# Kernel optimization log

Hardware: AMD Instinct MI355X
Metric: run time of the kernel (lower is better)

The kernel has to match this reference:

```python
import jax, jax.numpy as jnp
import numpy as np

B, C, H, W = 8, 512, 64, 64
DEPTH, HEADS = 4, 8


def setup_inputs() -> dict:
    key = jax.random.key(0)
    ks = jax.random.split(key, 7)
    s = 0.02
    return {
        "x": jax.random.normal(ks[0], (B, C, H, W), jnp.float32),
        # axial positional embeddings, emb dim at index 1: (1,C,H,1) and (1,C,1,W)
        "pos_h": jax.random.normal(ks[1], (C, H), jnp.float32) * s,
        "pos_w": jax.random.normal(ks[2], (C, W), jnp.float32) * s,
        # per layer, per axis (0=height, 1=width): q, kv, out projections
        "wq": jax.random.normal(ks[3], (DEPTH, 2, C, C), jnp.float32) * s,
        "wkv": jax.random.normal(ks[4], (DEPTH, 2, C, 2 * C), jnp.float32) * s,
        "wo": jax.random.normal(ks[5], (DEPTH, 2, C, C), jnp.float32) * s,
        "wo_b": jax.random.normal(ks[6], (DEPTH, 2, C), jnp.float32) * s,
    }


def _attn_last_axis(x, wq, wkv, wo, wo_b, heads):
    """Self-attention along the second-to-last axis. x: (..., L, C)."""
    lead = x.shape[:-2]
    L, Cd = x.shape[-2], x.shape[-1]
    e = Cd // heads
    q = x @ wq                       # (..., L, C)
    k, v = jnp.split(x @ wkv, 2, axis=-1)
    sh = lead + (L, heads, e)
    q, k, v = q.reshape(sh), k.reshape(sh), v.reshape(sh)
    dots = jnp.einsum('...ihe,...jhe->...hij', q, k) * (e ** -0.5)
    attn = jax.nn.softmax(dots, axis=-1)
    out = jnp.einsum('...hij,...jhe->...ihe', attn, v).reshape(lead + (L, heads * e))
    return out @ wo + wo_b


def reference(x, pos_h, pos_w, wq, wkv, wo, wo_b):
    # positional embedding: x + (1,C,H,1) + (1,C,1,W)
    x = x + pos_h[None, :, :, None] + pos_w[None, :, None, :]
    y = jnp.transpose(x, (0, 2, 3, 1))  # (B,H,W,C) channels-last working layout
    for l in range(DEPTH):
        # height-axis attention: (B,W,H,C), attend along H
        yh = jnp.transpose(y, (0, 2, 1, 3))
        oh = _attn_last_axis(yh, wq[l, 0], wkv[l, 0], wo[l, 0], wo_b[l, 0], HEADS)
        oh = jnp.transpose(oh, (0, 2, 1, 3))
        # width-axis attention: attend along W
        ow = _attn_last_axis(y, wq[l, 1], wkv[l, 1], wo[l, 1], wo_b[l, 1], HEADS)
        y = oh + ow  # sum_axial_out=True, no residual
    return jnp.transpose(y, (0, 3, 1, 2))  # back to (B,C,H,W)
```

## Files before the change

### kernel.cpp

```cpp
#include <hip/hip_runtime.h>
#include <stdint.h>


typedef __attribute__((ext_vector_type(8))) short bf16x8;
typedef __attribute__((ext_vector_type(4))) float f32x4;
typedef unsigned short u16;
typedef unsigned int u32;

#define MFMA16(a, b, c) __builtin_amdgcn_mfma_f32_16x16x32_bf16((a), (b), (c), 0, 0, 0)

__device__ __forceinline__ float b2f(u16 h) {
    u32 u = ((u32)h) << 16;
    float f;
    __builtin_memcpy(&f, &u, 4);
    return f;
}
__device__ __forceinline__ u16 f2b(float f) {
    u32 u;
    __builtin_memcpy(&u, &f, 4);
    u32 r = (u + 0x7fffu + ((u >> 16) & 1u)) >> 16;
    return (u16)r;
}

#define GLD_LDS16(g, l)                                                        \
    __builtin_amdgcn_global_load_lds(                                          \
        (const __attribute__((address_space(1))) void*)(g),                    \
        (__attribute__((address_space(3))) void*)(l), 16, 0, 0)

__global__ __launch_bounds__(256) void embed_kernel(
    const float* __restrict__ x, const float* __restrict__ ph,
    const float* __restrict__ pw, u16* __restrict__ y)
{
    __shared__ float tile[64][65];
    const int c0 = blockIdx.x * 64, h = blockIdx.y, b = blockIdx.z;
    const int t = threadIdx.x;
#pragma unroll
    for (int i = 0; i < 4; ++i) {
        int cl = (t >> 4) + i * 16;
        int w4 = (t & 15) * 4;
        const float* src = x + (((size_t)(b * 512 + c0 + cl)) * 64 + h) * 64 + w4;
        float4 v = *(const float4*)src;
        float p = ph[(c0 + cl) * 64 + h];
        tile[cl][w4 + 0] = v.x + p + pw[(c0 + cl) * 64 + w4 + 0];
        tile[cl][w4 + 1] = v.y + p + pw[(c0 + cl) * 64 + w4 + 1];
        tile[cl][w4 + 2] = v.z + p + pw[(c0 + cl) * 64 + w4 + 2];
        tile[cl][w4 + 3] = v.w + p + pw[(c0 + cl) * 64 + w4 + 3];
    }
    __syncthreads();
    const int wl = t >> 2, cb = (t & 3) * 16;
    bf16x8 o0, o1;
#pragma unroll
    for (int j = 0; j < 8; ++j) o0[j] = (short)f2b(tile[cb + j][wl]);
#pragma unroll
    for (int j = 0; j < 8; ++j) o1[j] = (short)f2b(tile[cb + 8 + j][wl]);
    u16* dst = y + (((size_t)(b * 64 + h) * 64 + wl) * 512 + c0 + cb);
    *(bf16x8*)dst = o0;
    *(bf16x8*)(dst + 8) = o1;
}

__global__ __launch_bounds__(256) void wtrans_kernel(
    const float* __restrict__ wq, const float* __restrict__ wkv,
    const float* __restrict__ wo, u16* __restrict__ wT)
{
    const int mid = blockIdx.z;
    const int l = mid / 6, rest = mid % 6, axis = rest / 3, which = rest % 3;
    const size_t la = (size_t)(l * 2 + axis);
    const float* src;
    int N;
    size_t doff;
    if (which == 0)      { src = wq  + la * 512 * 512;  N = 512;  doff = la * (2048 * 512); }
    else if (which == 1) { src = wkv + la * 512 * 1024; N = 1024; doff = la * (2048 * 512) + 512 * 512; }
    else                 { src = wo  + la * 512 * 512;  N = 512;  doff = la * (2048 * 512) + 512 * 512 + 1024 * 512; }
    const int n0 = blockIdx.y * 64;
    if (n0 >= N) return;
    const int k0 = blockIdx.x * 64;
    __shared__ float tile[64][65];
    const int t = threadIdx.x;
#pragma unroll
    for (int i = 0; i < 4; ++i) {
        int kl = (t >> 4) + i * 16;
        int n4 = (t & 15) * 4;
        float4 v = *(const float4*)(src + (size_t)(k0 + kl) * N + n0 + n4);
        tile[kl][n4 + 0] = v.x; tile[kl][n4 + 1] = v.y;
        tile[kl][n4 + 2] = v.z; tile[kl][n4 + 3] = v.w;
    }
    __syncthreads();
    const int nl = t >> 2, kb = (t & 3) * 16;
    bf16x8 o0, o1;
#pragma unroll
    for (int j = 0; j < 8; ++j) o0[j] = (short)f2b(tile[kb + j][nl]);
#pragma unroll
    for (int j = 0; j < 8; ++j) o1[j] = (short)f2b(tile[kb + 8 + j][nl]);
    u16* dst = wT + doff + (size_t)(n0 + nl) * 512 + k0 + kb;
    *(bf16x8*)dst = o0;
    *(bf16x8*)(dst + 8) = o1;
}

template <int MODE>
__global__ __launch_bounds__(256) void gemm_bt(
    const u16* __restrict__ A, int lda,
    const u16* __restrict__ Bt,
    const float* __restrict__ bias,
    u16* C, int ldc)
{
    __shared__ u16 As[128 * 64];
    __shared__ u16 Bs[128 * 64];
    const int tid = threadIdx.x;
    const int lane = tid & 63;
    const int wv = tid >> 6;
    const int wr = (wv >> 1) * 64, wc = (wv & 1) * 64;
    const int m0 = blockIdx.x * 128;
    const int n0 = blockIdx.y * 128;
    const int rl = lane >> 3;
    const int cp = lane & 7;
    const int l16 = lane & 15;
    const int kgrp = (lane >> 4) << 3;
    f32x4 acc[4][4] = {};

    for (int ks = 0; ks < 512; ks += 64) {
#pragma unroll
        for (int i = 0; i < 4; ++i) {
            int row = wv * 8 + i * 32 + rl;
            int clog = cp ^ (row & 7);
            const u16* src = A + (size_t)(m0 + row) * lda + ks + clog * 8;
            GLD_LDS16(src, As + (wv * 8 + i * 32) * 64);
        }
#pragma unroll
        for (int i = 0; i < 4; ++i) {
            int row = wv * 8 + i * 32 + rl;
            int clog = cp ^ (row & 7);
            const u16* src = Bt + (size_t)(n0 + row) * 512 + ks + clog * 8;
            GLD_LDS16(src, Bs + (wv * 8 + i * 32) * 64);
        }
        __syncthreads();
#pragma unroll
        for (int kk = 0; kk < 2; ++kk) {
            bf16x8 af[4], bfr[4];
            const int kb = (kk * 32 + kgrp) * 2;
#pragma unroll
            for (int mf = 0; mf < 4; ++mf) {
                int row = wr + mf * 16 + l16;
                af[mf] = *(const bf16x8*)((const char*)As + row * 128 + (kb ^ ((row & 7) << 4)));
            }
#pragma unroll
            for (int nf = 0; nf < 4; ++nf) {
                int row = wc + nf * 16 + l16;
                bfr[nf] = *(const bf16x8*)((const char*)Bs + row * 128 + (kb ^ ((row & 7) << 4)));
            }
#pragma unroll
            for (int mf = 0; mf < 4; ++mf)
#pragma unroll
                for (int nf = 0; nf < 4; ++nf)
                    acc[mf][nf] = MFMA16(af[mf], bfr[nf], acc[mf][nf]);
        }
        __syncthreads();
    }

    float bv[4];
    if (MODE >= 1) {
#pragma unroll
        for (int nf = 0; nf < 4; ++nf) bv[nf] = bias[n0 + wc + nf * 16 + l16];
    }
#pragma unroll
    for (int mf = 0; mf < 4; ++mf) {
#pragma unroll
        for (int r = 0; r < 4; ++r) {
            int m = m0 + wr + mf * 16 + ((lane >> 4) << 2) + r;
#pragma unroll
            for (int nf = 0; nf < 4; ++nf) {
                int n = n0 + wc + nf * 16 + l16;
                float v = acc[mf][nf][r];
                if (MODE >= 1) v += bv[nf];
                if (MODE == 2) v += b2f(C[(size_t)m * ldc + n]);
                C[(size_t)m * ldc + n] = f2b(v);
            }
        }
    }
}

__global__ __launch_bounds__(256) void attn_kernel(u16* QKV, int bstr, int tstr)
{
    __shared__ u16 sm[4][2][64 * 64];
    const int bi = blockIdx.x;
    const int base = (bi >> 6) * 4096 + (bi & 63) * bstr;
    const int tid = threadIdx.x, lane = tid & 63, wv = tid >> 6;
    const int l16 = lane & 15, kgrp = (lane >> 4) << 3;
    const int rl = lane >> 3, cp = lane & 7;
    u16* Kl = (u16*)sm[wv][0];
    u16* Vt = (u16*)sm[wv][1];

    for (int hh = 0; hh < 2; ++hh) {
        const int head = wv + hh * 4;
        const int hoff = head * 64;

        bf16x8 q[4][2];
#pragma unroll
        for (int mf = 0; mf < 4; ++mf)
#pragma unroll
            for (int k2 = 0; k2 < 2; ++k2) {
                const u16* p = QKV + (size_t)(base + (mf * 16 + l16) * tstr) * 1536
                             + hoff + k2 * 32 + kgrp;
                q[mf][k2] = *(const bf16x8*)p;
            }
        bf16x8 vvr[8];
#pragma unroll
        for (int i = 0; i < 8; ++i) {
            int j = i * 8 + rl;
            vvr[i] = *(const bf16x8*)(QKV + (size_t)(base + j * tstr) * 1536 + 1024 + hoff + cp * 8);
        }
#pragma unroll
        for (int i = 0; i < 8; ++i) {
            int row = i * 8 + rl;
            int clog = cp ^ (row & 7);
            const u16* src = QKV + (size_t)(base + row * tstr) * 1536 + 512 + hoff + clog * 8;
            GLD_LDS16(src, Kl + i * 8 * 64);
        }
        __syncthreads();

        f32x4 dt[4][4] = {};
#pragma unroll
        for (int k2 = 0; k2 < 2; ++k2) {
            bf16x8 bfr[4];
            const int kb = (k2 * 32 + kgrp) * 2;
#pragma unroll
            for (int jf = 0; jf < 4; ++jf) {
                int row = jf * 16 + l16;
                bfr[jf] = *(const bf16x8*)((const char*)Kl + row * 128 + (kb ^ ((row & 7) << 4)));
            }
#pragma unroll
            for (int mf = 0; mf < 4; ++mf)
#pragma unroll
                for (int jf = 0; jf < 4; ++jf)
                    dt[mf][jf] = MFMA16(q[mf][k2], bfr[jf], dt[mf][jf]);
        }

#pragma unroll
        for (int mf = 0; mf < 4; ++mf) {
#pragma unroll
            for (int r = 0; r < 4; ++r) {
                float a0 = dt[mf][0][r] * 0.125f, a1 = dt[mf][1][r] * 0.125f;
                float a2 = dt[mf][2][r] * 0.125f, a3 = dt[mf][3][r] * 0.125f;
                float mx = fmaxf(fmaxf(a0, a1), fmaxf(a2, a3));
#pragma unroll
                for (int msk = 1; msk < 16; msk <<= 1) mx = fmaxf(mx, __shfl_xor(mx, msk, 64));
                float e0 = __expf(a0 - mx), e1 = __expf(a1 - mx);
                float e2 = __expf(a2 - mx), e3 = __expf(a3 - mx);
                float sum = e0 + e1 + e2 + e3;
#pragma unroll
                for (int msk = 1; msk < 16; msk <<= 1) sum += __shfl_xor(sum, msk, 64);
                float inv = __builtin_amdgcn_rcpf(sum);
                dt[mf][0][r] = e0 * inv; dt[mf][1][r] = e1 * inv;
                dt[mf][2][r] = e2 * inv; dt[mf][3][r] = e3 * inv;
            }
        }

#pragma unroll
        for (int i = 0; i < 8; ++i) {
            int j = i * 8 + rl;
#pragma unroll
            for (int t = 0; t < 8; ++t) {
                int e = cp * 8 + t;
                int addr = e * 128 + 2 * j;
                *(u16*)((char*)Vt + (addr ^ ((e & 7) << 4))) = (u16)vvr[i][t];
            }
        }
#pragma unroll
        for (int mf = 0; mf < 4; ++mf)
#pragma unroll
            for (int r = 0; r < 4; ++r) {
                int irow = mf * 16 + ((lane >> 4) << 2) + r;
#pragma unroll
                for (int jf = 0; jf < 4; ++jf) {
                    int j = jf * 16 + l16;
                    int addr = irow * 128 + 2 * j;
                    *(u16*)((char*)Kl + (addr ^ ((irow & 7) << 4))) = f2b(dt[mf][jf][r]);
                }
            }

        f32x4 o[4][4] = {};
#pragma unroll
        for (int k2 = 0; k2 < 2; ++k2) {
            bf16x8 af[4], bfr[4];
            const int kb = (k2 * 32 + kgrp) * 2;
#pragma unroll
            for (int mf = 0; mf < 4; ++mf) {
                int row = mf * 16 + l16;
                af[mf] = *(const bf16x8*)((const char*)Kl + row * 128 + (kb ^ ((row & 7) << 4)));
            }
#pragma unroll
            for (int ef = 0; ef < 4; ++ef) {
                int row = ef * 16 + l16;
                bfr[ef] = *(const bf16x8*)((const char*)Vt + row * 128 + (kb ^ ((row & 7) << 4)));
            }
#pragma unroll
            for (int mf = 0; mf < 4; ++mf)
#pragma unroll
                for (int ef = 0; ef < 4; ++ef)
                    o[mf][ef] = MFMA16(af[mf], bfr[ef], o[mf][ef]);
        }

#pragma unroll
        for (int mf = 0; mf < 4; ++mf)
#pragma unroll
            for (int r = 0; r < 4; ++r) {
                int irow = mf * 16 + ((lane >> 4) << 2) + r;
                size_t rowoff = (size_t)(base + irow * tstr) * 1536;
#pragma unroll
                for (int ef = 0; ef < 4; ++ef) {
                    int e = ef * 16 + l16;
                    QKV[rowoff + hoff + e] = f2b(o[mf][ef][r]);
                }
            }
        __syncthreads();
    }
}

__global__ __launch_bounds__(256) void untrans_kernel(
    const u16* __restrict__ y, float* __restrict__ out)
{
    __shared__ float tile[64][65];
    const int c0 = blockIdx.x * 64, h = blockIdx.y, b = blockIdx.z;
    const int t = threadIdx.x;
    {
        const int wl = t >> 2, cb = (t & 3) * 16;
        const u16* src = y + (((size_t)(b * 64 + h) * 64 + wl) * 512 + c0 + cb);
        bf16x8 v0 = *(const bf16x8*)src;
        bf16x8 v1 = *(const bf16x8*)(src + 8);
#pragma unroll
        for (int j = 0; j < 8; ++j) tile[wl][cb + j] = b2f((u16)v0[j]);
#pragma unroll
        for (int j = 0; j < 8; ++j) tile[wl][cb + 8 + j] = b2f((u16)v1[j]);
    }
    __syncthreads();
    const int cl = t >> 2, w16 = (t & 3) * 16;
    float* dst = out + (((size_t)(b * 512 + c0 + cl)) * 64 + h) * 64 + w16;
#pragma unroll
    for (int j = 0; j < 4; ++j) {
        float4 v;
        v.x = tile[w16 + j * 4 + 0][cl];
        v.y = tile[w16 + j * 4 + 1][cl];
        v.z = tile[w16 + j * 4 + 2][cl];
        v.w = tile[w16 + j * 4 + 3][cl];
        *(float4*)(dst + j * 4) = v;
    }
}

extern "C" void kernel_launch(void* const* d_in, const int* in_sizes, int n_in,
                              void* d_out, int out_size, void* d_ws, size_t ws_size,
                              hipStream_t stream)
{
    (void)in_sizes; (void)n_in; (void)out_size; (void)ws_size;
    const float* x   = (const float*)d_in[0];
    const float* ph  = (const float*)d_in[1];
    const float* pw  = (const float*)d_in[2];
    const float* wq  = (const float*)d_in[3];
    const float* wkv = (const float*)d_in[4];
    const float* wo  = (const float*)d_in[5];
    const float* wob = (const float*)d_in[6];

    char* ws = (char*)d_ws;
    u16* yA  = (u16*)(ws);
    u16* yB  = (u16*)(ws + 33554432);
    u16* QKV = (u16*)(ws + 67108864);
    u16* wT  = (u16*)(ws + 167772160);
    float* out = (float*)d_out;

    embed_kernel<<<dim3(8, 64, 8), 256, 0, stream>>>(x, ph, pw, yA);
    wtrans_kernel<<<dim3(8, 16, 24), 256, 0, stream>>>(wq, wkv, wo, wT);

    u16* yin = yA;
    u16* yout = yB;
    for (int l = 0; l < 4; ++l) {
        for (int axis = 0; axis < 2; ++axis) {
            const u16* wTla = wT + (size_t)(l * 2 + axis) * 2048 * 512;
            const float* bias = wob + (size_t)(l * 2 + axis) * 512;
            gemm_bt<0><<<dim3(256, 12), 256, 0, stream>>>(yin, 512, wTla, nullptr, QKV, 1536);
            int bstr = (axis == 0) ? 1 : 64;
            int tstr = (axis == 0) ? 64 : 1;
            attn_kernel<<<dim3(512), 256, 0, stream>>>(QKV, bstr, tstr);
            const u16* woT = wTla + 512 * 512 + 1024 * 512;
            if (axis == 0)
                gemm_bt<1><<<dim3(256, 4), 256, 0, stream>>>(QKV, 1536, woT, bias, yout, 512);
            else
                gemm_bt<2><<<dim3(256, 4), 256, 0, stream>>>(QKV, 1536, woT, bias, yout, 512);
        }
        u16* tmp = yin; yin = yout; yout = tmp;
    }
    untrans_kernel<<<dim3(8, 64, 8), 256, 0, stream>>>(yin, out);
}
```

Before: 1.284 ms.

## Transpose MFMA operands for vectorized epilogues, XCD-aware block remap, and drop attention syncthreads

```diff
diff --git a/kernel.cpp b/kernel.cpp
--- a/kernel.cpp
+++ b/kernel.cpp
@@ -109,12 +109,17 @@
     const int lane = tid & 63;
     const int wv = tid >> 6;
     const int wr = (wv >> 1) * 64, wc = (wv & 1) * 64;
-    const int m0 = blockIdx.x * 128;
-    const int n0 = blockIdx.y * 128;
+    const int nbx = gridDim.x;
+    int lin = blockIdx.x + nbx * blockIdx.y;
+    int cpx = (nbx * gridDim.y) >> 3;
+    int id = (lin & 7) * cpx + (lin >> 3);
+    const int n0 = (id % nbx) * 128;
+    const int m0 = (id / nbx) * 128;
     const int rl = lane >> 3;
     const int cp = lane & 7;
     const int l16 = lane & 15;
-    const int kgrp = (lane >> 4) << 3;
+    const int g = lane >> 4;
+    const int kgrp = g << 3;
     f32x4 acc[4][4] = {};
 
     for (int ks = 0; ks < 512; ks += 64) {
@@ -148,32 +153,40 @@
                 bfr[nf] = *(const bf16x8*)((const char*)Bs + row * 128 + (kb ^ ((row & 7) << 4)));
             }
 #pragma unroll
-            for (int mf = 0; mf < 4; ++mf)
-#pragma unroll
-                for (int nf = 0; nf < 4; ++nf)
-                    acc[mf][nf] = MFMA16(af[mf], bfr[nf], acc[mf][nf]);
+            for (int nf = 0; nf < 4; ++nf)
+#pragma unroll
+                for (int mf = 0; mf < 4; ++mf)
+                    acc[nf][mf] = MFMA16(bfr[nf], af[mf], acc[nf][mf]);
         }
         __syncthreads();
     }
 
-    float bv[4];
+    float bv[4][4];
     if (MODE >= 1) {
 #pragma unroll
-        for (int nf = 0; nf < 4; ++nf) bv[nf] = bias[n0 + wc + nf * 16 + l16];
+        for (int nf = 0; nf < 4; ++nf) {
+            float4 b4 = *(const float4*)(bias + n0 + wc + nf * 16 + g * 4);
+            bv[nf][0] = b4.x; bv[nf][1] = b4.y; bv[nf][2] = b4.z; bv[nf][3] = b4.w;
+        }
     }
 #pragma unroll
     for (int mf = 0; mf < 4; ++mf) {
-#pragma unroll
-        for (int r = 0; r < 4; ++r) {
-            int m = m0 + wr + mf * 16 + ((lane >> 4) << 2) + r;
-#pragma unroll
-            for (int nf = 0; nf < 4; ++nf) {
-                int n = n0 + wc + nf * 16 + l16;
-                float v = acc[mf][nf][r];
-                if (MODE >= 1) v += bv[nf];
-                if (MODE == 2) v += b2f(C[(size_t)m * ldc + n]);
-                C[(size_t)m * ldc + n] = f2b(v);
-            }
+        const int m = m0 + wr + mf * 16 + l16;
+#pragma unroll
+        for (int nf = 0; nf < 4; ++nf) {
+            const int n = n0 + wc + nf * 16 + g * 4;
+            u16* cptr = C + (size_t)m * ldc + n;
+            float v0 = acc[nf][mf][0], v1 = acc[nf][mf][1];
+            float v2 = acc[nf][mf][2], v3 = acc[nf][mf][3];
+            if (MODE >= 1) { v0 += bv[nf][0]; v1 += bv[nf][1]; v2 += bv[nf][2]; v3 += bv[nf][3]; }
+            if (MODE == 2) {
+                ushort4 o = *(const ushort4*)cptr;
+                v0 += b2f(o.x); v1 += b2f(o.y); v2 += b2f(o.z); v3 += b2f(o.w);
+            }
+            uint2 pk;
+            pk.x = (u32)f2b(v0) | ((u32)f2b(v1) << 16);
+            pk.y = (u32)f2b(v2) | ((u32)f2b(v3) << 16);
+            *(uint2*)cptr = pk;
         }
     }
 }
@@ -184,7 +197,8 @@
     const int bi = blockIdx.x;
     const int base = (bi >> 6) * 4096 + (bi & 63) * bstr;
     const int tid = threadIdx.x, lane = tid & 63, wv = tid >> 6;
-    const int l16 = lane & 15, kgrp = (lane >> 4) << 3;
+    const int l16 = lane & 15, g = lane >> 4;
+    const int kgrp = g << 3;
     const int rl = lane >> 3, cp = lane & 7;
     u16* Kl = (u16*)sm[wv][0];
     u16* Vt = (u16*)sm[wv][1];
@@ -193,21 +207,6 @@
         const int head = wv + hh * 4;
         const int hoff = head * 64;
 
-        bf16x8 q[4][2];
-#pragma unroll
-        for (int mf = 0; mf < 4; ++mf)
-#pragma unroll
-            for (int k2 = 0; k2 < 2; ++k2) {
-                const u16* p = QKV + (size_t)(base + (mf * 16 + l16) * tstr) * 1536
-                             + hoff + k2 * 32 + kgrp;
-                q[mf][k2] = *(const bf16x8*)p;
-            }
-        bf16x8 vvr[8];
-#pragma unroll
-        for (int i = 0; i < 8; ++i) {
-            int j = i * 8 + rl;
-            vvr[i] = *(const bf16x8*)(QKV + (size_t)(base + j * tstr) * 1536 + 1024 + hoff + cp * 8);
-        }
 #pragma unroll
         for (int i = 0; i < 8; ++i) {
             int row = i * 8 + rl;
@@ -215,103 +214,124 @@
             const u16* src = QKV + (size_t)(base + row * tstr) * 1536 + 512 + hoff + clog * 8;
             GLD_LDS16(src, Kl + i * 8 * 64);
         }
-        __syncthreads();
-
-        f32x4 dt[4][4] = {};
+        bf16x8 q[4][2];
+#pragma unroll
+        for (int i_f = 0; i_f < 4; ++i_f)
+#pragma unroll
+            for (int k2 = 0; k2 < 2; ++k2)
+                q[i_f][k2] = *(const bf16x8*)(QKV + (size_t)(base + (i_f * 16 + l16) * tstr) * 1536
+                                              + hoff + k2 * 32 + kgrp);
+        bf16x8 vvr[8];
+#pragma unroll
+        for (int i = 0; i < 8; ++i)
+            vvr[i] = *(const bf16x8*)(QKV + (size_t)(base + (i * 8 + rl) * tstr) * 1536
+                                      + 1024 + hoff + cp * 8);
+
+        asm volatile("s_waitcnt vmcnt(0)" ::: "memory");
+        __builtin_amdgcn_sched_barrier(0);
+
+        f32x4 st[4][4] = {};
 #pragma unroll
         for (int k2 = 0; k2 < 2; ++k2) {
-            bf16x8 bfr[4];
+            bf16x8 kf[4];
             const int kb = (k2 * 32 + kgrp) * 2;
 #pragma unroll
-            for (int jf = 0; jf < 4; ++jf) {
-                int row = jf * 16 + l16;
-                bfr[jf] = *(const bf16x8*)((const char*)Kl + row * 128 + (kb ^ ((row & 7) << 4)));
-            }
-#pragma unroll
-            for (int mf = 0; mf < 4; ++mf)
-#pragma unroll
-                for (int jf = 0; jf < 4; ++jf)
-                    dt[mf][jf] = MFMA16(q[mf][k2], bfr[jf], dt[mf][jf]);
-        }
-
-#pragma unroll
-        for (int mf = 0; mf < 4; ++mf) {
-#pragma unroll
-            for (int r = 0; r < 4; ++r) {
-                float a0 = dt[mf][0][r] * 0.125f, a1 = dt[mf][1][r] * 0.125f;
-                float a2 = dt[mf][2][r] * 0.125f, a3 = dt[mf][3][r] * 0.125f;
-                float mx = fmaxf(fmaxf(a0, a1), fmaxf(a2, a3));
-#pragma unroll
-                for (int msk = 1; msk < 16; msk <<= 1) mx = fmaxf(mx, __shfl_xor(mx, msk, 64));
-                float e0 = __expf(a0 - mx), e1 = __expf(a1 - mx);
-                float e2 = __expf(a2 - mx), e3 = __expf(a3 - mx);
-                float sum = e0 + e1 + e2 + e3;
-#pragma unroll
-                for (int msk = 1; msk < 16; msk <<= 1) sum += __shfl_xor(sum, msk, 64);
-                float inv = __builtin_amdgcn_rcpf(sum);
-                dt[mf][0][r] = e0 * inv; dt[mf][1][r] = e1 * inv;
-                dt[mf][2][r] = e2 * inv; dt[mf][3][r] = e3 * inv;
-            }
+            for (int j_f = 0; j_f < 4; ++j_f) {
+                int row = j_f * 16 + l16;
+                kf[j_f] = *(const bf16x8*)((const char*)Kl + row * 128 + (kb ^ ((row & 7) << 4)));
+            }
+#pragma unroll
+            for (int i_f = 0; i_f < 4; ++i_f)
+#pragma unroll
+                for (int j_f = 0; j_f < 4; ++j_f)
+                    st[i_f][j_f] = MFMA16(kf[j_f], q[i_f][k2], st[i_f][j_f]);
         }
 
 #pragma unroll
         for (int i = 0; i < 8; ++i) {
-            int j = i * 8 + rl;
+            int j2 = i * 16 + rl * 2;
 #pragma unroll
             for (int t = 0; t < 8; ++t) {
                 int e = cp * 8 + t;
-                int addr = e * 128 + 2 * j;
-                *(u16*)((char*)Vt + (addr ^ ((e & 7) << 4))) = (u16)vvr[i][t];
-            }
-        }
-#pragma unroll
-        for (int mf = 0; mf < 4; ++mf)
-#pragma unroll
-            for (int r = 0; r < 4; ++r) {
-                int irow = mf * 16 + ((lane >> 4) << 2) + r;
-#pragma unroll
-                for (int jf = 0; jf < 4; ++jf) {
-                    int j = jf * 16 + l16;
-                    int addr = irow * 128 + 2 * j;
-                    *(u16*)((char*)Kl + (addr ^ ((irow & 7) << 4))) = f2b(dt[mf][jf][r]);
+                int addr = e * 128 + (j2 ^ (((t ^ cp) & 7) << 4));
+                *(u16*)((char*)Vt + addr) = (u16)vvr[i][t];
+            }
+        }
+
+#pragma unroll
+        for (int i_f = 0; i_f < 4; ++i_f) {
+            const int irow = i_f * 16 + l16;
+            float ev[4][4];
+            float mx = -1e30f;
+#pragma unroll
+            for (int j_f = 0; j_f < 4; ++j_f)
+#pragma unroll
+                for (int r = 0; r < 4; ++r) {
+                    float v = st[i_f][j_f][r] * 0.125f;
+                    ev[j_f][r] = v;
+                    mx = fmaxf(mx, v);
                 }
-            }
-
-        f32x4 o[4][4] = {};
+            mx = fmaxf(mx, __shfl_xor(mx, 16, 64));
+            mx = fmaxf(mx, __shfl_xor(mx, 32, 64));
+            float sum = 0.f;
+#pragma unroll
+            for (int j_f = 0; j_f < 4; ++j_f)
+#pragma unroll
+                for (int r = 0; r < 4; ++r) {
+                    float e = __expf(ev[j_f][r] - mx);
+                    ev[j_f][r] = e;
+                    sum += e;
+                }
+            sum += __shfl_xor(sum, 16, 64);
+            sum += __shfl_xor(sum, 32, 64);
+            float inv = __builtin_amdgcn_rcpf(sum);
+#pragma unroll
+            for (int j_f = 0; j_f < 4; ++j_f) {
+                uint2 pk;
+                pk.x = (u32)f2b(ev[j_f][0] * inv) | ((u32)f2b(ev[j_f][1] * inv) << 16);
+                pk.y = (u32)f2b(ev[j_f][2] * inv) | ((u32)f2b(ev[j_f][3] * inv) << 16);
+                int addr = irow * 128 + ((j_f * 32 + g * 8) ^ ((irow & 7) << 4));
+                *(uint2*)((char*)Kl + addr) = pk;
+            }
+        }
+
+        f32x4 of[4][4] = {};
 #pragma unroll
         for (int k2 = 0; k2 < 2; ++k2) {
-            bf16x8 af[4], bfr[4];
+            bf16x8 vf[4], pf[4];
             const int kb = (k2 * 32 + kgrp) * 2;
 #pragma unroll
-            for (int mf = 0; mf < 4; ++mf) {
-                int row = mf * 16 + l16;
-                af[mf] = *(const bf16x8*)((const char*)Kl + row * 128 + (kb ^ ((row & 7) << 4)));
-            }
-#pragma unroll
-            for (int ef = 0; ef < 4; ++ef) {
-                int row = ef * 16 + l16;
-                bfr[ef] = *(const bf16x8*)((const char*)Vt + row * 128 + (kb ^ ((row & 7) << 4)));
-            }
-#pragma unroll
-            for (int mf = 0; mf < 4; ++mf)
-#pragma unroll
-                for (int ef = 0; ef < 4; ++ef)
-                    o[mf][ef] = MFMA16(af[mf], bfr[ef], o[mf][ef]);
-        }
-
-#pragma unroll
-        for (int mf = 0; mf < 4; ++mf)
-#pragma unroll
-            for (int r = 0; r < 4; ++r) {
-                int irow = mf * 16 + ((lane >> 4) << 2) + r;
-                size_t rowoff = (size_t)(base + irow * tstr) * 1536;
-#pragma unroll
-                for (int ef = 0; ef < 4; ++ef) {
-                    int e = ef * 16 + l16;
-                    QKV[rowoff + hoff + e] = f2b(o[mf][ef][r]);
-                }
-            }
-        __syncthreads();
+            for (int e_f = 0; e_f < 4; ++e_f) {
+                int row = e_f * 16 + l16;
+                int sw = ((row & 7) ^ ((row >> 3) & 7)) << 4;
+                vf[e_f] = *(const bf16x8*)((const char*)Vt + row * 128 + (kb ^ sw));
+            }
+#pragma unroll
+            for (int i_f = 0; i_f < 4; ++i_f) {
+                int row = i_f * 16 + l16;
+                pf[i_f] = *(const bf16x8*)((const char*)Kl + row * 128 + (kb ^ ((row & 7) << 4)));
+            }
+#pragma unroll
+            for (int e_f = 0; e_f < 4; ++e_f)
+#pragma unroll
+                for (int i_f = 0; i_f < 4; ++i_f)
+                    of[e_f][i_f] = MFMA16(vf[e_f], pf[i_f], of[e_f][i_f]);
+        }
+
+#pragma unroll
+        for (int i_f = 0; i_f < 4; ++i_f) {
+            const int i = i_f * 16 + l16;
+            u16* orow = QKV + (size_t)(base + i * tstr) * 1536 + hoff + g * 4;
+#pragma unroll
+            for (int e_f = 0; e_f < 4; ++e_f) {
+                uint2 pk;
+                pk.x = (u32)f2b(of[e_f][i_f][0]) | ((u32)f2b(of[e_f][i_f][1]) << 16);
+                pk.y = (u32)f2b(of[e_f][i_f][2]) | ((u32)f2b(of[e_f][i_f][3]) << 16);
+                *(uint2*)(orow + e_f * 16) = pk;
+            }
+        }
+        asm volatile("s_waitcnt lgkmcnt(0)" ::: "memory");
+        __builtin_amdgcn_sched_barrier(0);
     }
 }
 
@@ -374,15 +394,15 @@
         for (int axis = 0; axis < 2; ++axis) {
             const u16* wTla = wT + (size_t)(l * 2 + axis) * 2048 * 512;
             const float* bias = wob + (size_t)(l * 2 + axis) * 512;
-            gemm_bt<0><<<dim3(256, 12), 256, 0, stream>>>(yin, 512, wTla, nullptr, QKV, 1536);
+            gemm_bt<0><<<dim3(12, 256), 256, 0, stream>>>(yin, 512, wTla, nullptr, QKV, 1536);
             int bstr = (axis == 0) ? 1 : 64;
             int tstr = (axis == 0) ? 64 : 1;
             attn_kernel<<<dim3(512), 256, 0, stream>>>(QKV, bstr, tstr);
             const u16* woT = wTla + 512 * 512 + 1024 * 512;
             if (axis == 0)
-                gemm_bt<1><<<dim3(256, 4), 256, 0, stream>>>(QKV, 1536, woT, bias, yout, 512);
+                gemm_bt<1><<<dim3(4, 256), 256, 0, stream>>>(QKV, 1536, woT, bias, yout, 512);
             else
-                gemm_bt<2><<<dim3(256, 4), 256, 0, stream>>>(QKV, 1536, woT, bias, yout, 512);
+                gemm_bt<2><<<dim3(4, 256), 256, 0, stream>>>(QKV, 1536, woT, bias, yout, 512);
         }
         u16* tmp = yin; yin = yout; yout = tmp;
     }
```

After: 1.233 ms. -4.0%, faster.
